# Kernel tuning notes

Hardware: AMD Instinct MI355X
Metric: run time of the kernel (lower is better)

Reference implementation:

```python
import jax, jax.numpy as jnp
import numpy as np

EPS_D = 1e-12  # clamp for sqrt of pairwise distances (diag is exactly 0)


def tr2dist_small(Y):
    # Y: (B, k, N) -> (B, N, N); standard protein-folding coords->distance map
    k = Y.shape[1]
    Z = Y - jnp.mean(Y, axis=2, keepdims=True)
    n2 = jnp.sum(Z * Z, axis=1)                        # (B, N)
    D = n2[:, None, :] + n2[:, :, None] - 2.0 * jnp.einsum('bkn,bkm->bnm', Z, Z)
    D = 3.0 * D / k
    return jnp.sqrt(jnp.maximum(D, EPS_D))


def mean_masked(X, mask, axis, keepdims=True):
    return jnp.sum(X * mask, axis=axis, keepdims=keepdims) / jnp.sum(mask, axis=axis, keepdims=keepdims)


def get_graph_lap(X, mask):
    # X: (B, C, N), mask: (B, 1, N)
    B, C, N = X.shape
    mm = jnp.einsum('bin,bim->bnm', mask, mask)        # (B, N, N) pair mask
    X = X - mean_masked(X, mask, axis=2) * mask
    X = X / jnp.sqrt(jnp.sum(X * X, axis=2, keepdims=True) / jnp.sum(mask, axis=2, keepdims=True) + 1e-4)
    pos = 0.5 * jnp.linspace(0.0, 1.0, N)[None, :] * mask   # (B, 1, N)
    Xa = jnp.concatenate((X, pos), axis=1)
    Wd = tr2dist_small(Xa) * mm
    sigma = mean_masked(Wd, mm, axis=(1, 2))           # (B, 1, 1)
    Wd = jnp.exp(-Wd / sigma * 10.0) * mm
    Wsum = jnp.sum(Wd, axis=1)                         # (B, N)
    L = jnp.zeros_like(Wd) + Wsum[:, :, None] * jnp.eye(N, dtype=Wd.dtype)[None] - Wd
    L = 0.5 * (L + jnp.swapaxes(L, 1, 2))
    return L, Wd


def _forward(Z, mask, K0, Knet, W, Wend):
    h = 0.01
    m = mask[:, None, :]                               # (B, 1, N)
    Z = jnp.tanh(jnp.einsum('oc,bcn->bon', K0, Z)) * m
    nlayers = W.shape[0]
    for i in range(nlayers):
        L, _ = get_graph_lap(Z, m)
        Ki = Knet[i]
        Wi = W[i, :, :, :, 0]                          # (3, C, C) size-1 kernels
        cv = lambda w, x: jnp.einsum('oc,bcn->bon', w, x) * m     # conv1d, k=1
        cvT = lambda w, x: jnp.einsum('co,bcn->bon', w, x) * m    # conv_transpose1d, k=1
        mm1 = lambda x: jnp.einsum('bcn,bnm->bcm', x, L)
        Ai = Ki[0] * cv(Wi[0], Z) + mm1(Ki[1] * cv(Wi[1], Z)) + mm1(mm1(Ki[2] * cv(Wi[2], Z)))
        Ai = (Ai - mean_masked(Ai, m, axis=2)) * m
        Ai = Ai / jnp.sqrt(jnp.sum(Ai * Ai, axis=1, keepdims=True) + 0.001)
        Ai = jax.nn.relu(Ai)
        Ai = Ki[0] * cvT(Wi[0], Ai) + mm1(Ki[1] * cvT(Wi[1], Ai)) + mm1(mm1(Ki[2] * cvT(Wi[2], Ai)))
        Z = Z - h * Ai
    Zout = jnp.einsum('oc,bcn->bon', Wend[:, :, 0], Z) * m       # (B, chan_out, N)
    dists = tuple(tr2dist_small(Zout[:, 3 * i:3 * i + 3, :]) for i in range(Zout.shape[1] // 3))
    return dists + (Zout,)


def setup_inputs() -> dict:
    key = jax.random.key(0)
    ks = jax.random.split(key, 6)
    B, chan_in, chan_out, channels, N, nlayers = 16, 40, 3, 256, 1024, 6
    stdv0 = 0.1 * channels / chan_in
    return {
        'Z': jax.random.normal(ks[0], (B, chan_in, N), dtype=jnp.float32),
        'mask': jnp.ones((B, N), dtype=jnp.float32),
        'K0': jax.random.uniform(ks[1], (channels, chan_in), minval=-stdv0, maxval=stdv0, dtype=jnp.float32),
        'Knet': jax.random.uniform(ks[2], (nlayers, chan_out), minval=-stdv0, maxval=stdv0, dtype=jnp.float32),
        'W': jax.random.uniform(ks[3], (nlayers, 3, channels, channels, 1), minval=-0.1, maxval=0.1, dtype=jnp.float32),
        'Wend': 1e-4 * jax.random.normal(ks[4], (chan_out, channels, 1), dtype=jnp.float32),
    }


def reference(Z, mask, K0, Knet, W, Wend):
    return _forward(Z, mask, K0, Knet, W, Wend)
```

## Files before the change

kernel.cpp:

```cpp
#include <hip/hip_runtime.h>
#include <hip/hip_fp16.h>
#include <math.h>

#define BB 16
#define CIN 40
#define CH 256
#define NN 1024
#define NLAYERS 6

typedef unsigned short ush;
typedef __attribute__((ext_vector_type(8))) short bh8;
typedef __attribute__((ext_vector_type(8))) _Float16 h8;
typedef __attribute__((ext_vector_type(4))) float f4;

__device__ __forceinline__ ush bf16_rne(float x) {
  unsigned int u = __float_as_uint(x);
  u += 0x7fffu + ((u >> 16) & 1u);
  return (ush)(u >> 16);
}
__device__ __forceinline__ float bf16_f(ush h) {
  return __uint_as_float(((unsigned int)h) << 16);
}
__device__ __forceinline__ ush f2h(float x) {
  __half h = __float2half(x);
  return *(ush*)&h;
}
__device__ __forceinline__ float h2f(ush u) {
  __half h = *(__half*)&u;
  return __half2float(h);
}
__device__ __forceinline__ float fast_tanh(float x) {
  const float e = __expf(2.0f * x);
  return (e - 1.0f) / (e + 1.0f);
}

#define GLD16(gp, lp) __builtin_amdgcn_global_load_lds( \
    (const __attribute__((address_space(1))) void*)(gp), \
    (__attribute__((address_space(3))) void*)(lp), 16, 0, 0)

__device__ __forceinline__ float blockReduceSum(float v) {
  __shared__ float sred[4];
  const int lane = threadIdx.x & 63;
  const int wid  = threadIdx.x >> 6;
  #pragma unroll
  for (int off = 32; off > 0; off >>= 1) v += __shfl_down(v, off, 64);
  __syncthreads();
  if (lane == 0) sred[wid] = v;
  __syncthreads();
  return sred[0] + sred[1] + sred[2] + sred[3];
}

__device__ __forceinline__ void stageA(
    const ush* __restrict__ Ah, const ush* __restrict__ Al, const int sA,
    const ush* __restrict__ Bh, const ush* __restrict__ Bl, const int sB,
    const int kt, ush* buf) {
  const int lane = threadIdx.x & 63;
  const int wid = threadIdx.x >> 6;
  const int srow = lane >> 2;
  const int sl = (lane & 3) ^ ((srow >> 1) & 3);
  #pragma unroll
  for (int cc = 0; cc < 8; cc++) {
    const int c = wid * 8 + cc;
    const ush* src;
    if (c < 8)       src = Ah + (size_t)(c * 16 + srow) * sA + kt + sl * 8;
    else if (c < 16) src = Al + (size_t)((c - 8) * 16 + srow) * sA + kt + sl * 8;
    else if (c < 24) src = Bh + (size_t)((c - 16) * 16 + srow) * sB + kt + sl * 8;
    else             src = Bl + (size_t)((c - 24) * 16 + srow) * sB + kt + sl * 8;
    GLD16(src, buf + c * 512 + lane * 8);
  }
}

__device__ __forceinline__ void computeA(const ush* buf, f4 acc[4][4]) {
  const int lane = threadIdx.x & 63;
  const int wid = threadIdx.x >> 6;
  const int wr = wid >> 1, wc = wid & 1;
  const int frow = lane & 15;
  const int slot8 = (((lane >> 4) ^ ((frow >> 1) & 3)) << 3);
  bh8 ah[4], al[4], bh_[4], bl_[4];
  #pragma unroll
  for (int mi = 0; mi < 4; mi++) {
    const int off = (wr * 64 + mi * 16 + frow) * 32 + slot8;
    ah[mi] = *(const bh8*)&buf[off];
    al[mi] = *(const bh8*)&buf[4096 + off];
  }
  #pragma unroll
  for (int ni = 0; ni < 4; ni++) {
    const int off = (wc * 64 + ni * 16 + frow) * 32 + slot8;
    bh_[ni] = *(const bh8*)&buf[8192 + off];
    bl_[ni] = *(const bh8*)&buf[12288 + off];
  }
  #pragma unroll
  for (int mi = 0; mi < 4; mi++)
    #pragma unroll
    for (int ni = 0; ni < 4; ni++) {
      acc[mi][ni] = __builtin_amdgcn_mfma_f32_16x16x32_bf16(ah[mi], bh_[ni], acc[mi][ni], 0, 0, 0);
      acc[mi][ni] = __builtin_amdgcn_mfma_f32_16x16x32_bf16(ah[mi], bl_[ni], acc[mi][ni], 0, 0, 0);
      acc[mi][ni] = __builtin_amdgcn_mfma_f32_16x16x32_bf16(al[mi], bh_[ni], acc[mi][ni], 0, 0, 0);
    }
}

__device__ __forceinline__ void stageCV(
    const ush* __restrict__ Ap, const int sA,
    const ush* __restrict__ Bh, const ush* __restrict__ Bl, const int sB,
    const int kt, ush* buf) {
  const int lane = threadIdx.x & 63;
  const int wid = threadIdx.x >> 6;
  const int srow = lane >> 2;
  const int sl = (lane & 3) ^ ((srow >> 1) & 3);
  #pragma unroll
  for (int cc = 0; cc < 6; cc++) {
    const int c = wid * 6 + cc;
    const ush* src;
    if (c < 8)       src = Ap + (size_t)(c * 16 + srow) * sA + kt + sl * 8;
    else if (c < 16) src = Bh + (size_t)((c - 8) * 16 + srow) * sB + kt + sl * 8;
    else             src = Bl + (size_t)((c - 16) * 16 + srow) * sB + kt + sl * 8;
    GLD16(src, buf + c * 512 + lane * 8);
  }
}

__device__ __forceinline__ void computeCV(const ush* buf, f4 acc[4][4]) {
  const int lane = threadIdx.x & 63;
  const int wid = threadIdx.x >> 6;
  const int wr = wid >> 1, wc = wid & 1;
  const int frow = lane & 15;
  const int slot8 = (((lane >> 4) ^ ((frow >> 1) & 3)) << 3);
  h8 a_[4], bh_[4], bl_[4];
  #pragma unroll
  for (int mi = 0; mi < 4; mi++) {
    const int off = (wr * 64 + mi * 16 + frow) * 32 + slot8;
    a_[mi] = *(const h8*)&buf[off];
  }
  #pragma unroll
  for (int ni = 0; ni < 4; ni++) {
    const int off = (wc * 64 + ni * 16 + frow) * 32 + slot8;
    bh_[ni] = *(const h8*)&buf[4096 + off];
    bl_[ni] = *(const h8*)&buf[8192 + off];
  }
  #pragma unroll
  for (int mi = 0; mi < 4; mi++)
    #pragma unroll
    for (int ni = 0; ni < 4; ni++) {
      acc[mi][ni] = __builtin_amdgcn_mfma_f32_16x16x32_f16(a_[mi], bh_[ni], acc[mi][ni], 0, 0, 0);
      acc[mi][ni] = __builtin_amdgcn_mfma_f32_16x16x32_f16(a_[mi], bl_[ni], acc[mi][ni], 0, 0, 0);
    }
}

__device__ __forceinline__ void stageMM(
    const ush* __restrict__ Ah, const ush* __restrict__ Al, const int sA,
    const ush* __restrict__ Bp, const int sB, const int kt, ush* buf) {
  const int lane = threadIdx.x & 63;
  const int wid = threadIdx.x >> 6;
  const int srow = lane >> 2;
  const int sl = (lane & 3) ^ ((srow >> 1) & 3);
  #pragma unroll
  for (int cc = 0; cc < 4; cc++) {
    const int c = wid * 4 + cc;
    const ush* src;
    if (c < 4)       src = Ah + (size_t)(c * 16 + srow) * sA + kt + sl * 8;
    else if (c < 8)  src = Al + (size_t)((c - 4) * 16 + srow) * sA + kt + sl * 8;
    else             src = Bp + (size_t)((c - 8) * 16 + srow) * sB + kt + sl * 8;
    GLD16(src, buf + c * 512 + lane * 8);
  }
}

__device__ __forceinline__ void computeMM(const ush* buf, f4 acc[4][2]) {
  const int lane = threadIdx.x & 63;
  const int wid = threadIdx.x >> 6;
  const int frow = lane & 15;
  const int slot8 = (((lane >> 4) ^ ((frow >> 1) & 3)) << 3);
  h8 ah[4], al[4], b_[2];
  #pragma unroll
  for (int mi = 0; mi < 4; mi++) {
    const int off = (mi * 16 + frow) * 32 + slot8;
    ah[mi] = *(const h8*)&buf[off];
    al[mi] = *(const h8*)&buf[2048 + off];
  }
  #pragma unroll
  for (int ni = 0; ni < 2; ni++) {
    const int off = (wid * 32 + ni * 16 + frow) * 32 + slot8;
    b_[ni] = *(const h8*)&buf[4096 + off];
  }
  #pragma unroll
  for (int mi = 0; mi < 4; mi++)
    #pragma unroll
    for (int ni = 0; ni < 2; ni++) {
      acc[mi][ni] = __builtin_amdgcn_mfma_f32_16x16x32_f16(ah[mi], b_[ni], acc[mi][ni], 0, 0, 0);
      acc[mi][ni] = __builtin_amdgcn_mfma_f32_16x16x32_f16(al[mi], b_[ni], acc[mi][ni], 0, 0, 0);
    }
}

__global__ void k0_kernel(const float* __restrict__ Zin, const float* __restrict__ K0,
                          const float* __restrict__ mask, float* __restrict__ Zc,
                          float* __restrict__ statS1, float* __restrict__ statS2) {
  const int b = blockIdx.y;
  const int o = blockIdx.x;
  __shared__ float w[CIN];
  if (threadIdx.x < CIN) w[threadIdx.x] = K0[o * CIN + threadIdx.x];
  __syncthreads();
  float s1 = 0.f, s2 = 0.f;
  for (int n = threadIdx.x; n < NN; n += 256) {
    float acc = 0.f;
    #pragma unroll
    for (int c = 0; c < CIN; c++) acc += w[c] * Zin[((size_t)b * CIN + c) * NN + n];
    const float z = fast_tanh(acc) * mask[b * NN + n];
    Zc[((size_t)b * CH + o) * NN + n] = z;
    s1 += z; s2 += z * z;
  }
  s1 = blockReduceSum(s1);
  s2 = blockReduceSum(s2);
  if (threadIdx.x == 0) {
    const size_t base = ((size_t)b * CH + o) * 8;
    statS1[base] = s1; statS2[base] = s2;
    #pragma unroll
    for (int k = 1; k < 8; k++) { statS1[base + k] = 0.f; statS2[base + k] = 0.f; }
  }
}

__global__ void masksum_kernel(const float* __restrict__ mask, float* __restrict__ msum,
                               float* __restrict__ posv) {
  const int b = blockIdx.x;
  float v = 0.f, p = 0.f;
  for (int n = threadIdx.x; n < NN; n += 256) {
    const float m = mask[b * NN + n];
    v += m;
    p += 0.5f * ((float)n * (1.0f / (NN - 1))) * m;
  }
  v = blockReduceSum(v);
  p = blockReduceSum(p);
  const float pm = p * (1.0f / NN);
  if (threadIdx.x == 0) msum[b] = v;
  for (int n = threadIdx.x; n < NN; n += 256)
    posv[b * NN + n] = 0.5f * ((float)n * (1.0f / (NN - 1))) * mask[b * NN + n] - pm;
}

__global__ void wprep_kernel(const float* __restrict__ W, ush* __restrict__ Wm,
                             ush* __restrict__ Wt) {
  __shared__ float t[64][65];
  const int mat = blockIdx.y;
  const int ty = blockIdx.x >> 2, tx = blockIdx.x & 3;
  const float* src = W + (size_t)mat * CH * CH;
  const int tid = threadIdx.x;
  const int lr = tid >> 2;
  const int lc = (tid & 3) * 16;
  float v[16];
  #pragma unroll
  for (int j = 0; j < 16; j += 4)
    *(float4*)&v[j] = *(const float4*)&src[(size_t)(ty * 64 + lr) * CH + tx * 64 + lc + j];
  ush hv[16];
  #pragma unroll
  for (int j = 0; j < 16; j++) {
    hv[j] = f2h(v[j]);
    t[lr][lc + j] = v[j];
  }
  const size_t offm = (size_t)mat * CH * CH + (size_t)(ty * 64 + lr) * CH + tx * 64 + lc;
  #pragma unroll
  for (int j = 0; j < 16; j += 4)
    *(ushort4*)&Wm[offm + j] = *(ushort4*)&hv[j];
  __syncthreads();
  #pragma unroll
  for (int j = 0; j < 16; j++) hv[j] = f2h(t[lc + j][lr]);
  const size_t offt = (size_t)mat * CH * CH + (size_t)(tx * 64 + lr) * CH + ty * 64 + lc;
  #pragma unroll
  for (int j = 0; j < 16; j += 4)
    *(ushort4*)&Wt[offt + j] = *(ushort4*)&hv[j];
}

__global__ void tsplitZ_kernel(const float* __restrict__ in, ush* __restrict__ Th,
                               ush* __restrict__ Tl) {
  __shared__ float t[32][65];
  const int b = blockIdx.z;
  const int n0 = blockIdx.x * 64;
  const int k0 = blockIdx.y * 32;
  const float* src = in + (size_t)b * CH * NN;
  const int tid = threadIdx.x;
  const int lr = tid >> 3;
  const int lc = (tid & 7) * 8;
  const int gk = k0 + lr;
  *(float4*)&t[lr][lc]     = *(const float4*)&src[(size_t)gk * NN + n0 + lc];
  *(float4*)&t[lr][lc + 4] = *(const float4*)&src[(size_t)gk * NN + n0 + lc + 4];
  __syncthreads();
  const int on = tid >> 2;
  const int ok = (tid & 3) * 8;
  ush hv[8], lv[8];
  #pragma unroll
  for (int j = 0; j < 8; j++) {
    const float v = t[ok + j][on];
    hv[j] = f2h(v); lv[j] = f2h(v - h2f(hv[j]));
  }
  const size_t off = ((size_t)b * NN + n0 + on) * CH + k0 + ok;
  *(ushort4*)&Th[off] = *(ushort4*)&hv[0];
  *(ushort4*)&Th[off + 4] = *(ushort4*)&hv[4];
  *(ushort4*)&Tl[off] = *(ushort4*)&lv[0];
  *(ushort4*)&Tl[off + 4] = *(ushort4*)&lv[4];
}

__global__ void tsplitY2_kernel(const ush* __restrict__ Zsh, const ush* __restrict__ Zsl,
                                const float* __restrict__ mask,
                                const float* __restrict__ statS1, const float* __restrict__ statS2,
                                const float* __restrict__ msum, ush* __restrict__ Th,
                                ush* __restrict__ Tl, float* __restrict__ n2part) {
  __shared__ float smu[32], srs[32];
  const int b = blockIdx.z;
  const int n0 = blockIdx.x * 64;
  const int k0 = blockIdx.y * 32;
  const int tid = threadIdx.x;
  if (tid < 32) {
    const size_t base = ((size_t)b * CH + k0 + tid) * 8;
    float S1 = 0.f, S2 = 0.f;
    #pragma unroll
    for (int k = 0; k < 8; k++) { S1 += statS1[base + k]; S2 += statS2[base + k]; }
    const float M = msum[b];
    const float mu = S1 / M;
    const float q = fmaxf(S2 - mu * S1, 0.f);
    smu[tid] = mu;
    srs[tid] = 1.0f / sqrtf(q / M + 1e-4f);
  }
  __syncthreads();
  const int n = n0 + (tid >> 2);
  const int kl = (tid & 3) * 8;
  const int kc = k0 + kl;
  const float mn = mask[b * NN + n];
  const size_t zoff = ((size_t)b * NN + n) * CH + kc;
  const ushort4 h0 = *(const ushort4*)&Zsh[zoff];
  const ushort4 h1 = *(const ushort4*)&Zsh[zoff + 4];
  const ushort4 l0 = *(const ushort4*)&Zsl[zoff];
  const ushort4 l1 = *(const ushort4*)&Zsl[zoff + 4];
  float val[8];
  val[0] = (h2f(h0.x) + h2f(l0.x) - smu[kl + 0] * mn) * srs[kl + 0];
  val[1] = (h2f(h0.y) + h2f(l0.y) - smu[kl + 1] * mn) * srs[kl + 1];
  val[2] = (h2f(h0.z) + h2f(l0.z) - smu[kl + 2] * mn) * srs[kl + 2];
  val[3] = (h2f(h0.w) + h2f(l0.w) - smu[kl + 3] * mn) * srs[kl + 3];
  val[4] = (h2f(h1.x) + h2f(l1.x) - smu[kl + 4] * mn) * srs[kl + 4];
  val[5] = (h2f(h1.y) + h2f(l1.y) - smu[kl + 5] * mn) * srs[kl + 5];
  val[6] = (h2f(h1.z) + h2f(l1.z) - smu[kl + 6] * mn) * srs[kl + 6];
  val[7] = (h2f(h1.w) + h2f(l1.w) - smu[kl + 7] * mn) * srs[kl + 7];
  float s = 0.f;
  ush hv[8], lv[8];
  #pragma unroll
  for (int j = 0; j < 8; j++) {
    s += val[j] * val[j];
    hv[j] = bf16_rne(val[j]);
    lv[j] = bf16_rne(val[j] - bf16_f(hv[j]));
  }
  const size_t off = ((size_t)b * NN + n) * CH + kc;
  *(ushort4*)&Th[off] = *(ushort4*)&hv[0];
  *(ushort4*)&Th[off + 4] = *(ushort4*)&hv[4];
  *(ushort4*)&Tl[off] = *(ushort4*)&lv[0];
  *(ushort4*)&Tl[off + 4] = *(ushort4*)&lv[4];
  s += __shfl_xor(s, 1, 64);
  s += __shfl_xor(s, 2, 64);
  if ((tid & 3) == 0) n2part[((size_t)b * 8 + blockIdx.y) * NN + n] = s;
}

__global__ __launch_bounds__(256, 2)
void gram_v6_kernel(const ush* __restrict__ Yth, const ush* __restrict__ Ytl,
                    const float* __restrict__ n2part, const float* __restrict__ mask,
                    const float* __restrict__ posv, ush* __restrict__ Dp,
                    float* __restrict__ sigpart) {
  __shared__ ush lds[32768];
  __shared__ float sn2[256];
  __shared__ float spv[256];
  const int bid = blockIdx.x;
  const int logical = (bid & 7) * 72 + (bid >> 3);
  const int b = logical / 36;
  int t = logical - b * 36;
  int ty = 0;
  while (t >= 8 - ty) { t -= 8 - ty; ++ty; }
  const int tx = ty + t;
  const int i0 = ty * 128;
  const int j0 = tx * 128;
  {
    const int tt = threadIdx.x;
    const int nn = (tt < 128) ? (i0 + tt) : (j0 + tt - 128);
    const float pv = posv[b * NN + nn];
    float s = pv * pv;
    #pragma unroll
    for (int kb = 0; kb < 8; kb++) s += n2part[((size_t)b * 8 + kb) * NN + nn];
    sn2[tt] = s;
    spv[tt] = pv;
  }
  const ush* Ah = Yth + (size_t)b * NN * CH + (size_t)i0 * CH;
  const ush* Al = Ytl + (size_t)b * NN * CH + (size_t)i0 * CH;
  const ush* Bh = Yth + (size_t)b * NN * CH + (size_t)j0 * CH;
  const ush* Bl = Ytl + (size_t)b * NN * CH + (size_t)j0 * CH;
  f4 acc[4][4];
  const f4 z4 = {0.f, 0.f, 0.f, 0.f};
  #pragma unroll
  for (int mi = 0; mi < 4; mi++)
    #pragma unroll
    for (int ni = 0; ni < 4; ni++) acc[mi][ni] = z4;
  stageA(Ah, Al, CH, Bh, Bl, CH, 0, lds);
  __syncthreads();
  int pb = 0;
  for (int kt = 32; kt < CH; kt += 32) {
    stageA(Ah, Al, CH, Bh, Bl, CH, kt, lds + (pb ^ 1) * 16384);
    computeA(lds + pb * 16384, acc);
    __syncthreads();
    pb ^= 1;
  }
  computeA(lds + pb * 16384, acc);
  const int lane = threadIdx.x & 63;
  const int wid = threadIdx.x >> 6;
  const int wr = wid >> 1, wc = wid & 1;
  const int frow = lane & 15, hh = lane >> 4;
  const float scale = 3.0f / 257.0f;
  float lsum = 0.f;
  #pragma unroll
  for (int ni = 0; ni < 4; ni++) {
    const int jl = wc * 64 + ni * 16 + frow;
    const int j = j0 + jl;
    const float n2j = sn2[128 + jl];
    const float pj = spv[128 + jl];
    const float mkj = mask[b * NN + j];
    #pragma unroll
    for (int mi = 0; mi < 4; mi++) {
      const int il = wr * 64 + mi * 16 + hh * 4;
      ush dv[4];
      #pragma unroll
      for (int r = 0; r < 4; r++) {
        const int i = i0 + il + r;
        const float g = acc[mi][ni][r] + spv[il + r] * pj;
        const float D = scale * (sn2[il + r] + n2j - 2.0f * g);
        const float d = sqrtf(fmaxf(D, 1e-12f));
        const float mmv = mask[b * NN + i] * mkj;
        const float wd = d * mmv;
        lsum += wd * mmv;
        dv[r] = f2h(wd);
      }
      if (ty != tx) {
        uint2 mr;
        mr.x = (unsigned)dv[0] | ((unsigned)dv[1] << 16);
        mr.y = (unsigned)dv[2] | ((unsigned)dv[3] << 16);
        *(uint2*)&Dp[((size_t)b * NN + j) * NN + i0 + il] = mr;
      }
      #pragma unroll
      for (int r = 0; r < 4; r++) {
        const unsigned v = dv[r];
        const unsigned vp = (unsigned)__shfl_xor((int)v, 1, 64);
        if ((frow & 1) == 0)
          *(unsigned*)&Dp[((size_t)b * NN + i0 + il + r) * NN + j] = v | (vp << 16);
      }
    }
  }
  if (ty != tx) lsum *= 2.0f;
  #pragma unroll
  for (int off = 32; off > 0; off >>= 1) lsum += __shfl_down(lsum, off, 64);
  __syncthreads();
  float* rbuf = (float*)lds;
  if (lane == 0) rbuf[wid] = lsum;
  __syncthreads();
  if (threadIdx.x == 0)
    sigpart[(size_t)b * 64 + ty * 8 + tx] = rbuf[0] + rbuf[1] + rbuf[2] + rbuf[3];
}

__global__ void expw4_kernel(const ush* __restrict__ Dp, const float* __restrict__ mask,
                             const float* __restrict__ sigpart, const float* __restrict__ msum,
                             ush* __restrict__ Wp) {
  __shared__ float sfb;
  const int b = blockIdx.y, n = blockIdx.x;
  const int t = threadIdx.x;
  {
    float v = 0.f;
    if (t < 64) {
      const int sy = t >> 3, sx = t & 7;
      if (sy <= sx) v = sigpart[b * 64 + t];
    }
    v = blockReduceSum(v);
    if (t == 0) { const float ms = msum[b]; sfb = -10.0f * ms * ms / v; }
  }
  __syncthreads();
  const float fb = sfb;
  const float mn = mask[b * NN + n];
  const size_t roff = ((size_t)b * NN + n) * NN;
  const float4 mk = ((const float4*)(mask + b * NN))[t];
  const ushort4 dp = *(const ushort4*)&Dp[roff + t * 4];
  const float w0 = __expf(fb * h2f(dp.x)) * mn * mk.x;
  const float w1 = __expf(fb * h2f(dp.y)) * mn * mk.y;
  const float w2 = __expf(fb * h2f(dp.z)) * mn * mk.z;
  const float w3 = __expf(fb * h2f(dp.w)) * mn * mk.w;
  const float s = blockReduceSum(w0 + w1 + w2 + w3);
  float v0 = -w0, v1 = -w1, v2 = -w2, v3 = -w3;
  if ((n >> 2) == t) {
    const int r = n & 3;
    if (r == 0) v0 += s; else if (r == 1) v1 += s; else if (r == 2) v2 += s; else v3 += s;
  }
  ushort4 h4;
  h4.x = f2h(v0); h4.y = f2h(v1); h4.z = f2h(v2); h4.w = f2h(v3);
  *(ushort4*)&Wp[roff + t * 4] = h4;
}

__global__ __launch_bounds__(256, 3)
void cvall_kernel(const ush* __restrict__ Ap, const ush* __restrict__ Bth,
                  const ush* __restrict__ Btl, const float* __restrict__ mask,
                  const float* __restrict__ Kis, unsigned int* __restrict__ Cpack,
                  ush* __restrict__ C2h, ush* __restrict__ C2l) {
  __shared__ ush lds[24576];
  const int bid = blockIdx.x;
  const int logical = (bid & 7) * 96 + (bid >> 3);
  const int b = logical / 48;
  const int inner = logical - b * 48;
  const int c0g = inner & 7;
  const int r0g = inner >> 3;
  const int r0 = r0g * 128;
  const int c0 = c0g * 128;
  const ush* Aq = Ap + (size_t)r0 * CH;
  const ush* Bh = Bth + (size_t)b * NN * CH + (size_t)c0 * CH;
  const ush* Bl = Btl + (size_t)b * NN * CH + (size_t)c0 * CH;
  f4 acc[4][4];
  const f4 z4 = {0.f, 0.f, 0.f, 0.f};
  #pragma unroll
  for (int mi = 0; mi < 4; mi++)
    #pragma unroll
    for (int ni = 0; ni < 4; ni++) acc[mi][ni] = z4;
  stageCV(Aq, CH, Bh, Bl, CH, 0, lds);
  __syncthreads();
  int pb = 0;
  for (int kt = 32; kt < CH; kt += 32) {
    stageCV(Aq, CH, Bh, Bl, CH, kt, lds + (pb ^ 1) * 12288);
    computeCV(lds + pb * 12288, acc);
    __syncthreads();
    pb ^= 1;
  }
  computeCV(lds + pb * 12288, acc);
  const int lane = threadIdx.x & 63;
  const int wid = threadIdx.x >> 6;
  const int wr = wid >> 1, wc = wid & 1;
  const int frow = lane & 15, hh = lane >> 4;
  const float alpha = Kis[r0g >> 1];
  #pragma unroll
  for (int ni = 0; ni < 4; ni++) {
    const int jl = wc * 64 + ni * 16 + frow;
    const int col = c0 + jl;
    const float am = alpha * mask[b * NN + col];
    #pragma unroll
    for (int mi = 0; mi < 4; mi++) {
      const int il = wr * 64 + mi * 16 + hh * 4;
      #pragma unroll
      for (int r = 0; r < 4; r++) {
        const int row = r0 + il + r;
        const float v = acc[mi][ni][r] * am;
        const ush h = f2h(v);
        const ush l = f2h(v - h2f(h));
        const unsigned pv = (unsigned)h | ((unsigned)l << 16);
        const unsigned pvp = (unsigned)__shfl_xor((int)pv, 1, 64);
        if ((frow & 1) == 0) {
          if (r0g < 4) {
            uint2 w2; w2.x = pv; w2.y = pvp;
            *(uint2*)&Cpack[((size_t)b * 512 + row) * NN + col] = w2;
          } else {
            const size_t obase = ((size_t)b * 256 + (row - 512)) * NN + col;
            const unsigned hw = (pv & 0xffffu) | (pvp << 16);
            const unsigned lw = (pv >> 16) | (pvp & 0xffff0000u);
            *(unsigned*)&C2h[obase] = hw;
            *(unsigned*)&C2l[obase] = lw;
          }
        }
      }
    }
  }
}

template <int OUTMODE, int STATS>
__global__ __launch_bounds__(256, 5)
void mm1_v6_kernel(const ush* __restrict__ Xh, const ush* __restrict__ Xl, const size_t xStride,
                   const ush* __restrict__ Wp,
                   const unsigned int* __restrict__ addp, const size_t aStride,
                   const float* __restrict__ zin, const float* __restrict__ mask,
                   float* __restrict__ outF, ush* __restrict__ outH, ush* __restrict__ outL,
                   float* __restrict__ statS1, float* __restrict__ statS2) {
  __shared__ ush lds[16384];
  const int bid = blockIdx.x;
  const int logical = (bid & 7) * 64 + (bid >> 3);
  const int b = logical >> 5;
  const int inner = logical & 31;
  const int n0 = (inner & 7) * 128;
  const int r0 = (inner >> 3) * 64;
  const ush* Ah = Xh + (size_t)b * xStride + (size_t)r0 * NN;
  const ush* Al = Xl + (size_t)b * xStride + (size_t)r0 * NN;
  const ush* Bp = Wp + (size_t)b * NN * NN + (size_t)n0 * NN;
  f4 acc[4][2];
  const f4 z4 = {0.f, 0.f, 0.f, 0.f};
  #pragma unroll
  for (int mi = 0; mi < 4; mi++) { acc[mi][0] = z4; acc[mi][1] = z4; }
  stageMM(Ah, Al, NN, Bp, NN, 0, lds);
  __syncthreads();
  int pb = 0;
  for (int kt = 32; kt < NN; kt += 32) {
    stageMM(Ah, Al, NN, Bp, NN, kt, lds + (pb ^ 1) * 8192);
    computeMM(lds + pb * 8192, acc);
    __syncthreads();
    pb ^= 1;
  }
  computeMM(lds + pb * 8192, acc);
  const int lane = threadIdx.x & 63;
  const int wid = threadIdx.x >> 6;
  const int frow = lane & 15, hh = lane >> 4;
  float a1[4][4];
  float a2[4][4];
  if (STATS) {
    #pragma unroll
    for (int mi = 0; mi < 4; mi++)
      #pragma unroll
      for (int r = 0; r < 4; r++) { a1[mi][r] = 0.f; a2[mi][r] = 0.f; }
  }
  __syncthreads();
  unsigned int* tl = (unsigned int*)lds;
  #pragma unroll
  for (int ni = 0; ni < 2; ni++) {
    const int jl = wid * 32 + ni * 16 + frow;
    const int col = n0 + jl;
    const float mk = STATS ? mask[b * NN + col] : 0.f;
    #pragma unroll
    for (int mi = 0; mi < 4; mi++) {
      const int il = mi * 16 + hh * 4;
      unsigned int pv[4];
      #pragma unroll
      for (int r = 0; r < 4; r++) {
        const int row = r0 + il + r;
        const unsigned int av = addp[(size_t)b * aStride + (size_t)row * NN + col];
        const float o = acc[mi][ni][r] + h2f((ush)(av & 0xffffu)) + h2f((ush)(av >> 16));
        float val;
        if (OUTMODE == 2) {
          const size_t ooff = (size_t)b * CH * NN + (size_t)row * NN + col;
          val = zin[ooff] - 0.01f * o;
          outF[ooff] = val;
        } else {
          val = o;
        }
        if (STATS) { a1[mi][r] += val * mk; a2[mi][r] += val * val * mk; }
        const ush h = f2h(val);
        const ush l = f2h(val - h2f(h));
        pv[r] = (unsigned int)h | ((unsigned int)l << 16);
      }
      const int slot = (il >> 2) ^ (jl & 15);
      *(uint4*)&tl[jl * 64 + slot * 4] = *(uint4*)pv;
    }
  }
  __syncthreads();
  if (OUTMODE == 0) {
    const int rrow = threadIdx.x >> 2;
    const int rch = (threadIdx.x & 3) * 32;
    const size_t obase = ((size_t)b * 256 + r0 + rrow) * NN + n0 + rch;
    #pragma unroll
    for (int g = 0; g < 4; g++) {
      unsigned int hw[4], lw[4];
      #pragma unroll
      for (int q = 0; q < 4; q++) {
        unsigned int h2[2], l2[2];
        #pragma unroll
        for (int e = 0; e < 2; e++) {
          const int jl = rch + g * 8 + q * 2 + e;
          const int slot = (rrow >> 2) ^ (jl & 15);
          const unsigned int v = tl[jl * 64 + slot * 4 + (rrow & 3)];
          h2[e] = v & 0xffffu; l2[e] = v >> 16;
        }
        hw[q] = h2[0] | (h2[1] << 16);
        lw[q] = l2[0] | (l2[1] << 16);
      }
      *(uint4*)&outH[obase + g * 8] = *(uint4*)hw;
      *(uint4*)&outL[obase + g * 8] = *(uint4*)lw;
    }
  } else {
    const int nloc = threadIdx.x >> 1;
    const int ch0 = (threadIdx.x & 1) * 32;
    #pragma unroll
    for (int half = 0; half < 2; half++) {
      unsigned int hw[8], lw[8];
      #pragma unroll
      for (int q = 0; q < 8; q++) {
        const int ila = ch0 + half * 16 + q * 2;
        const int ilb = ila + 1;
        const unsigned int va = tl[nloc * 64 + (((ila >> 2) ^ (nloc & 15)) << 2) + (ila & 3)];
        const unsigned int vb = tl[nloc * 64 + (((ilb >> 2) ^ (nloc & 15)) << 2) + (ilb & 3)];
        hw[q] = (va & 0xffffu) | (vb << 16);
        lw[q] = (va >> 16) | (vb & 0xffff0000u);
      }
      const size_t zoff = ((size_t)b * NN + n0 + nloc) * CH + r0 + ch0 + half * 16;
      *(uint4*)&outH[zoff] = *(uint4*)&hw[0];
      *(uint4*)&outH[zoff + 8] = *(uint4*)&hw[4];
      *(uint4*)&outL[zoff] = *(uint4*)&lw[0];
      *(uint4*)&outL[zoff + 8] = *(uint4*)&lw[4];
    }
  }
  if (STATS) {
    #pragma unroll
    for (int mi = 0; mi < 4; mi++)
      #pragma unroll
      for (int r = 0; r < 4; r++) {
        #pragma unroll
        for (int d = 1; d < 16; d <<= 1) {
          a1[mi][r] += __shfl_xor(a1[mi][r], d, 64);
          a2[mi][r] += __shfl_xor(a2[mi][r], d, 64);
        }
      }
    __syncthreads();
    float* s1b = (float*)lds;
    float* s2b = s1b + 256;
    if (frow == 0) {
      #pragma unroll
      for (int mi = 0; mi < 4; mi++)
        #pragma unroll
        for (int r = 0; r < 4; r++) {
          const int row = mi * 16 + hh * 4 + r;
          s1b[wid * 64 + row] = a1[mi][r];
          s2b[wid * 64 + row] = a2[mi][r];
        }
    }
    __syncthreads();
    if (threadIdx.x < 64) {
      const int row = threadIdx.x;
      const float p1 = s1b[row] + s1b[64 + row] + s1b[128 + row] + s1b[192 + row];
      const float p2 = s2b[row] + s2b[64 + row] + s2b[128 + row] + s2b[192 + row];
      const int nblk = n0 >> 7;
      statS1[((size_t)b * CH + r0 + row) * 8 + nblk] = p1;
      statS2[((size_t)b * CH + r0 + row) * 8 + nblk] = p2;
    }
  }
}

__global__ void csq_kernel(const ush* __restrict__ Uh, const ush* __restrict__ Ul,
                           const float* __restrict__ mask, const float* __restrict__ statS1,
                           const float* __restrict__ msum, float* __restrict__ part) {
  __shared__ float srm[16];
  const int b = blockIdx.y, cc = blockIdx.x;
  if (threadIdx.x < 16) {
    const size_t base = ((size_t)b * CH + cc * 16 + threadIdx.x) * 8;
    float S1 = 0.f;
    #pragma unroll
    for (int k = 0; k < 8; k++) S1 += statS1[base + k];
    srm[threadIdx.x] = S1 / msum[b];
  }
  __syncthreads();
  const int n = threadIdx.x * 4;
  const float4 m4 = *(const float4*)&mask[b * NN + n];
  float4 s4 = {0.f, 0.f, 0.f, 0.f};
  for (int r = 0; r < 16; r++) {
    const int c = cc * 16 + r;
    const float rm = srm[r];
    const size_t uoff = ((size_t)b * 256 + c) * NN + n;
    const ushort4 uh = *(const ushort4*)&Uh[uoff];
    const ushort4 ul = *(const ushort4*)&Ul[uoff];
    float a;
    a = (h2f(uh.x) + h2f(ul.x) - rm) * m4.x; s4.x += a * a;
    a = (h2f(uh.y) + h2f(ul.y) - rm) * m4.y; s4.y += a * a;
    a = (h2f(uh.z) + h2f(ul.z) - rm) * m4.z; s4.z += a * a;
    a = (h2f(uh.w) + h2f(ul.w) - rm) * m4.w; s4.w += a * a;
  }
  *(float4*)&part[((size_t)(b * 16 + cc)) * NN + n] = s4;
}

__global__ void tsplitN2_kernel(const ush* __restrict__ Uh, const ush* __restrict__ Ul,
                                const float* __restrict__ mask, const float* __restrict__ statS1,
                                const float* __restrict__ msum, const float* __restrict__ part,
                                ush* __restrict__ Th, ush* __restrict__ Tl) {
  __shared__ float t[32][65];
  __shared__ float srm[32];
  __shared__ float srsl[64];
  const int b = blockIdx.z;
  const int n0 = blockIdx.x * 64;
  const int k0 = blockIdx.y * 32;
  const int tid = threadIdx.x;
  if (tid < 32) {
    const size_t base = ((size_t)b * CH + k0 + tid) * 8;
    float S1 = 0.f;
    #pragma unroll
    for (int k = 0; k < 8; k++) S1 += statS1[base + k];
    srm[tid] = S1 / msum[b];
  } else if (tid < 96) {
    const int n = n0 + tid - 32;
    float s = 0.001f;
    #pragma unroll
    for (int cc = 0; cc < 16; cc++) s += part[((size_t)(b * 16 + cc)) * NN + n];
    srsl[tid - 32] = 1.0f / sqrtf(s);
  }
  __syncthreads();
  const int lr = tid >> 3;
  const int lc = (tid & 7) * 8;
  const int gc = k0 + lr;
  const float rm = srm[lr];
  const float4 ma = *(const float4*)&mask[b * NN + n0 + lc];
  const float4 mb = *(const float4*)&mask[b * NN + n0 + lc + 4];
  const size_t uoff = ((size_t)b * 256 + gc) * NN + n0 + lc;
  const ushort4 ha = *(const ushort4*)&Uh[uoff];
  const ushort4 hb = *(const ushort4*)&Uh[uoff + 4];
  const ushort4 la = *(const ushort4*)&Ul[uoff];
  const ushort4 lb = *(const ushort4*)&Ul[uoff + 4];
  t[lr][lc + 0] = fmaxf((h2f(ha.x) + h2f(la.x) - rm) * ma.x * srsl[lc + 0], 0.f);
  t[lr][lc + 1] = fmaxf((h2f(ha.y) + h2f(la.y) - rm) * ma.y * srsl[lc + 1], 0.f);
  t[lr][lc + 2] = fmaxf((h2f(ha.z) + h2f(la.z) - rm) * ma.z * srsl[lc + 2], 0.f);
  t[lr][lc + 3] = fmaxf((h2f(ha.w) + h2f(la.w) - rm) * ma.w * srsl[lc + 3], 0.f);
  t[lr][lc + 4] = fmaxf((h2f(hb.x) + h2f(lb.x) - rm) * mb.x * srsl[lc + 4], 0.f);
  t[lr][lc + 5] = fmaxf((h2f(hb.y) + h2f(lb.y) - rm) * mb.y * srsl[lc + 5], 0.f);
  t[lr][lc + 6] = fmaxf((h2f(hb.z) + h2f(lb.z) - rm) * mb.z * srsl[lc + 6], 0.f);
  t[lr][lc + 7] = fmaxf((h2f(hb.w) + h2f(lb.w) - rm) * mb.w * srsl[lc + 7], 0.f);
  __syncthreads();
  const int on = tid >> 2;
  const int ok = (tid & 3) * 8;
  ush hv[8], lv[8];
  #pragma unroll
  for (int j = 0; j < 8; j++) {
    const float v = t[ok + j][on];
    hv[j] = f2h(v); lv[j] = f2h(v - h2f(hv[j]));
  }
  const size_t off = ((size_t)b * NN + n0 + on) * CH + k0 + ok;
  *(ushort4*)&Th[off] = *(ushort4*)&hv[0];
  *(ushort4*)&Th[off + 4] = *(ushort4*)&hv[4];
  *(ushort4*)&Tl[off] = *(ushort4*)&lv[0];
  *(ushort4*)&Tl[off + 4] = *(ushort4*)&lv[4];
}

__global__ void zout_kernel(const float* __restrict__ Z, const float* __restrict__ Wend,
                            const float* __restrict__ mask, float* __restrict__ outZ,
                            float* __restrict__ Zcent) {
  const int b = blockIdx.x;
  __shared__ float w[3 * CH];
  for (int i = threadIdx.x; i < 3 * CH; i += 256) w[i] = Wend[i];
  __syncthreads();
  float a[3][4];
  #pragma unroll
  for (int j = 0; j < 4; j++) { a[0][j] = 0.f; a[1][j] = 0.f; a[2][j] = 0.f; }
  const float* Zb = Z + (size_t)b * CH * NN;
  for (int c = 0; c < CH; c++) {
    const float w0 = w[c], w1 = w[CH + c], w2 = w[2 * CH + c];
    #pragma unroll
    for (int j = 0; j < 4; j++) {
      float zv = Zb[(size_t)c * NN + threadIdx.x + j * 256];
      a[0][j] += w0 * zv; a[1][j] += w1 * zv; a[2][j] += w2 * zv;
    }
  }
  float sum[3] = {0.f, 0.f, 0.f};
  #pragma unroll
  for (int j = 0; j < 4; j++) {
    const int n = threadIdx.x + j * 256;
    const float mv = mask[b * NN + n];
    #pragma unroll
    for (int o = 0; o < 3; o++) {
      a[o][j] *= mv;
      outZ[((size_t)b * 3 + o) * NN + n] = a[o][j];
      sum[o] += a[o][j];
    }
  }
  for (int o = 0; o < 3; o++) {
    float s = blockReduceSum(sum[o]);
    const float mean = s * (1.0f / NN);
    #pragma unroll
    for (int j = 0; j < 4; j++) {
      const int n = threadIdx.x + j * 256;
      Zcent[((size_t)b * 3 + o) * NN + n] = a[o][j] - mean;
    }
  }
}

__global__ void dist_kernel(const float* __restrict__ Zcent, float* __restrict__ outD) {
  const int b = blockIdx.z;
  const int n = blockIdx.y;
  const int m = blockIdx.x * 256 + threadIdx.x;
  const float* Zb = Zcent + (size_t)b * 3 * NN;
  const float x0 = Zb[n], x1 = Zb[NN + n], x2 = Zb[2 * NN + n];
  const float d0 = x0 - Zb[m], d1 = x1 - Zb[NN + m], d2 = x2 - Zb[2 * NN + m];
  const float D = d0 * d0 + d1 * d1 + d2 * d2;
  outD[((size_t)b * NN + n) * NN + m] = sqrtf(fmaxf(D, 1e-12f));
}

extern "C" void kernel_launch(void* const* d_in, const int* in_sizes, int n_in,
                              void* d_out, int out_size, void* d_ws, size_t ws_size,
                              hipStream_t stream) {
  const float* Zin  = (const float*)d_in[0];
  const float* mask = (const float*)d_in[1];
  const float* K0   = (const float*)d_in[2];
  const float* Knet = (const float*)d_in[3];
  const float* W    = (const float*)d_in[4];
  const float* Wend = (const float*)d_in[5];
  float* out = (float*)d_out;

  ush* Wp = (ush*)out;
  ush* Dp = Wp + (size_t)BB * NN * NN;
  float* outZ = out + (size_t)BB * NN * NN;

  float* p = (float*)d_ws;
  float* uni = p; p += (size_t)BB * 768 * NN;
  ush* Yth = (ush*)uni;
  ush* Ytl = Yth + (size_t)BB * NN * CH;
  unsigned int* Cpack = (unsigned int*)uni;
  ush* C2h = (ush*)(uni + (size_t)BB * 512 * NN);
  ush* C2l = C2h + (size_t)BB * 256 * NN;

  float* Zcur = p; p += (size_t)BB * CH * NN;
  ush* Thb = (ush*)p; p += (size_t)BB * NN * CH / 2;
  ush* Tlb = (ush*)p; p += (size_t)BB * NN * CH / 2;
  ush* Zsh = (ush*)p; p += (size_t)BB * NN * CH / 2;
  ush* Zsl = (ush*)p; p += (size_t)BB * NN * CH / 2;
  ush* Wm = (ush*)p; p += (size_t)18 * CH * CH / 2;
  ush* Wt = (ush*)p; p += (size_t)18 * CH * CH / 2;
  float* msum  = p; p += BB;
  float* posv  = p; p += BB * NN;
  float* sigp  = p; p += BB * 64;
  float* statS1= p; p += (size_t)BB * CH * 8;
  float* statS2= p; p += (size_t)BB * CH * 8;
  float* n2part= p; p += (size_t)BB * 8 * NN;
  float* partb = p; p += (size_t)BB * 16 * NN;
  float* Zcent = p; p += BB * 3 * NN;

  const dim3 gtsZ(NN / 64, CH / 32, BB);
  const size_t sC = (size_t)512 * NN;
  const size_t sT = (size_t)CH * NN;

  masksum_kernel<<<BB, 256, 0, stream>>>(mask, msum, posv);
  wprep_kernel<<<dim3(16, 18), 256, 0, stream>>>(W, Wm, Wt);
  k0_kernel<<<dim3(CH, BB), 256, 0, stream>>>(Zin, K0, mask, Zcur, statS1, statS2);
  tsplitZ_kernel<<<gtsZ, 256, 0, stream>>>(Zcur, Zsh, Zsl);

  for (int layer = 0; layer < NLAYERS; layer++) {
    tsplitY2_kernel<<<gtsZ, 256, 0, stream>>>(Zsh, Zsl, mask, statS1, statS2, msum,
                                              Yth, Ytl, n2part);
    gram_v6_kernel<<<576, 256, 0, stream>>>(Yth, Ytl, n2part, mask, posv, Dp, sigp);
    expw4_kernel<<<dim3(NN, BB), 256, 0, stream>>>(Dp, mask, sigp, msum, Wp);

    const ush* Am = Wm + (size_t)layer * 3 * CH * CH;
    const ush* At = Wt + (size_t)layer * 3 * CH * CH;
    const float* Ki = Knet + layer * 3;

    cvall_kernel<<<768, 256, 0, stream>>>(Am, Zsh, Zsl, mask, Ki, Cpack, C2h, C2l);
    mm1_v6_kernel<0, 0><<<512, 256, 0, stream>>>(C2h, C2l, sT, Wp,
        Cpack + (size_t)256 * NN, sC, nullptr, nullptr, nullptr, Thb, Tlb, nullptr, nullptr);
    mm1_v6_kernel<0, 1><<<512, 256, 0, stream>>>(Thb, Tlb, sT, Wp,
        Cpack, sC, nullptr, mask, nullptr, C2h, C2l, statS1, statS2);

    csq_kernel<<<dim3(16, BB), 256, 0, stream>>>(C2h, C2l, mask, statS1, msum, partb);
    tsplitN2_kernel<<<gtsZ, 256, 0, stream>>>(C2h, C2l, mask, statS1, msum, partb, Thb, Tlb);

    cvall_kernel<<<768, 256, 0, stream>>>(At, Thb, Tlb, mask, Ki, Cpack, C2h, C2l);
    mm1_v6_kernel<0, 0><<<512, 256, 0, stream>>>(C2h, C2l, sT, Wp,
        Cpack + (size_t)256 * NN, sC, nullptr, nullptr, nullptr, Thb, Tlb, nullptr, nullptr);
    mm1_v6_kernel<2, 1><<<512, 256, 0, stream>>>(Thb, Tlb, sT, Wp,
        Cpack, sC, Zcur, mask, Zcur, Zsh, Zsl, statS1, statS2);
  }

  zout_kernel<<<BB, 256, 0, stream>>>(Zcur, Wend, mask, outZ, Zcent);
  dist_kernel<<<dim3(NN / 256, NN, BB), 256, 0, stream>>>(Zcent, out);
}
```

Baseline: 1.770 ms.

## Use fp16 hi/lo split for Gram kernel, drop low B term; batch k0 outputs

```diff
diff --git a/kernel.cpp b/kernel.cpp
--- a/kernel.cpp
+++ b/kernel.cpp
@@ -13,14 +13,6 @@
 typedef __attribute__((ext_vector_type(8))) _Float16 h8;
 typedef __attribute__((ext_vector_type(4))) float f4;
 
-__device__ __forceinline__ ush bf16_rne(float x) {
-  unsigned int u = __float_as_uint(x);
-  u += 0x7fffu + ((u >> 16) & 1u);
-  return (ush)(u >> 16);
-}
-__device__ __forceinline__ float bf16_f(ush h) {
-  return __uint_as_float(((unsigned int)h) << 16);
-}
 __device__ __forceinline__ ush f2h(float x) {
   __half h = __float2half(x);
   return *(ush*)&h;
@@ -50,52 +42,48 @@
   return sred[0] + sred[1] + sred[2] + sred[3];
 }
 
-__device__ __forceinline__ void stageA(
-    const ush* __restrict__ Ah, const ush* __restrict__ Al, const int sA,
-    const ush* __restrict__ Bh, const ush* __restrict__ Bl, const int sB,
-    const int kt, ush* buf) {
+__device__ __forceinline__ void stageG(
+    const ush* __restrict__ Ah, const ush* __restrict__ Al,
+    const ush* __restrict__ Bh, const int s, const int kt, ush* buf) {
   const int lane = threadIdx.x & 63;
   const int wid = threadIdx.x >> 6;
   const int srow = lane >> 2;
   const int sl = (lane & 3) ^ ((srow >> 1) & 3);
   #pragma unroll
-  for (int cc = 0; cc < 8; cc++) {
-    const int c = wid * 8 + cc;
+  for (int cc = 0; cc < 6; cc++) {
+    const int c = wid * 6 + cc;
     const ush* src;
-    if (c < 8)       src = Ah + (size_t)(c * 16 + srow) * sA + kt + sl * 8;
-    else if (c < 16) src = Al + (size_t)((c - 8) * 16 + srow) * sA + kt + sl * 8;
-    else if (c < 24) src = Bh + (size_t)((c - 16) * 16 + srow) * sB + kt + sl * 8;
-    else             src = Bl + (size_t)((c - 24) * 16 + srow) * sB + kt + sl * 8;
+    if (c < 8)       src = Ah + (size_t)(c * 16 + srow) * s + kt + sl * 8;
+    else if (c < 16) src = Al + (size_t)((c - 8) * 16 + srow) * s + kt + sl * 8;
+    else             src = Bh + (size_t)((c - 16) * 16 + srow) * s + kt + sl * 8;
     GLD16(src, buf + c * 512 + lane * 8);
   }
 }
 
-__device__ __forceinline__ void computeA(const ush* buf, f4 acc[4][4]) {
+__device__ __forceinline__ void computeG(const ush* buf, f4 acc[4][4]) {
   const int lane = threadIdx.x & 63;
   const int wid = threadIdx.x >> 6;
   const int wr = wid >> 1, wc = wid & 1;
   const int frow = lane & 15;
   const int slot8 = (((lane >> 4) ^ ((frow >> 1) & 3)) << 3);
-  bh8 ah[4], al[4], bh_[4], bl_[4];
+  h8 ah[4], al[4], b_[4];
   #pragma unroll
   for (int mi = 0; mi < 4; mi++) {
     const int off = (wr * 64 + mi * 16 + frow) * 32 + slot8;
-    ah[mi] = *(const bh8*)&buf[off];
-    al[mi] = *(const bh8*)&buf[4096 + off];
+    ah[mi] = *(const h8*)&buf[off];
+    al[mi] = *(const h8*)&buf[4096 + off];
   }
   #pragma unroll
   for (int ni = 0; ni < 4; ni++) {
     const int off = (wc * 64 + ni * 16 + frow) * 32 + slot8;
-    bh_[ni] = *(const bh8*)&buf[8192 + off];
-    bl_[ni] = *(const bh8*)&buf[12288 + off];
+    b_[ni] = *(const h8*)&buf[8192 + off];
   }
   #pragma unroll
   for (int mi = 0; mi < 4; mi++)
     #pragma unroll
     for (int ni = 0; ni < 4; ni++) {
-      acc[mi][ni] = __builtin_amdgcn_mfma_f32_16x16x32_bf16(ah[mi], bh_[ni], acc[mi][ni], 0, 0, 0);
-      acc[mi][ni] = __builtin_amdgcn_mfma_f32_16x16x32_bf16(ah[mi], bl_[ni], acc[mi][ni], 0, 0, 0);
-      acc[mi][ni] = __builtin_amdgcn_mfma_f32_16x16x32_bf16(al[mi], bh_[ni], acc[mi][ni], 0, 0, 0);
+      acc[mi][ni] = __builtin_amdgcn_mfma_f32_16x16x32_f16(ah[mi], b_[ni], acc[mi][ni], 0, 0, 0);
+      acc[mi][ni] = __builtin_amdgcn_mfma_f32_16x16x32_f16(al[mi], b_[ni], acc[mi][ni], 0, 0, 0);
     }
 }
 
@@ -193,26 +181,38 @@
                           const float* __restrict__ mask, float* __restrict__ Zc,
                           float* __restrict__ statS1, float* __restrict__ statS2) {
   const int b = blockIdx.y;
-  const int o = blockIdx.x;
-  __shared__ float w[CIN];
-  if (threadIdx.x < CIN) w[threadIdx.x] = K0[o * CIN + threadIdx.x];
-  __syncthreads();
-  float s1 = 0.f, s2 = 0.f;
+  const int o0 = blockIdx.x * 8;
+  __shared__ float w[8][CIN];
+  for (int i = threadIdx.x; i < 8 * CIN; i += 256)
+    w[i / CIN][i % CIN] = K0[(o0 + i / CIN) * CIN + i % CIN];
+  __syncthreads();
+  float s1[8], s2[8];
+  #pragma unroll
+  for (int o = 0; o < 8; o++) { s1[o] = 0.f; s2[o] = 0.f; }
   for (int n = threadIdx.x; n < NN; n += 256) {
-    float acc = 0.f;
-    #pragma unroll
-    for (int c = 0; c < CIN; c++) acc += w[c] * Zin[((size_t)b * CIN + c) * NN + n];
-    const float z = fast_tanh(acc) * mask[b * NN + n];
-    Zc[((size_t)b * CH + o) * NN + n] = z;
-    s1 += z; s2 += z * z;
-  }
-  s1 = blockReduceSum(s1);
-  s2 = blockReduceSum(s2);
-  if (threadIdx.x == 0) {
-    const size_t base = ((size_t)b * CH + o) * 8;
-    statS1[base] = s1; statS2[base] = s2;
-    #pragma unroll
-    for (int k = 1; k < 8; k++) { statS1[base + k] = 0.f; statS2[base + k] = 0.f; }
+    float zv[CIN];
+    #pragma unroll
+    for (int c = 0; c < CIN; c++) zv[c] = Zin[((size_t)b * CIN + c) * NN + n];
+    const float mn = mask[b * NN + n];
+    #pragma unroll
+    for (int o = 0; o < 8; o++) {
+      float acc = 0.f;
+      #pragma unroll
+      for (int c = 0; c < CIN; c++) acc += w[o][c] * zv[c];
+      const float z = fast_tanh(acc) * mn;
+      Zc[((size_t)b * CH + o0 + o) * NN + n] = z;
+      s1[o] += z; s2[o] += z * z;
+    }
+  }
+  for (int o = 0; o < 8; o++) {
+    const float r1 = blockReduceSum(s1[o]);
+    const float r2 = blockReduceSum(s2[o]);
+    if (threadIdx.x == 0) {
+      const size_t base = ((size_t)b * CH + o0 + o) * 8;
+      statS1[base] = r1; statS2[base] = r2;
+      #pragma unroll
+      for (int k = 1; k < 8; k++) { statS1[base + k] = 0.f; statS2[base + k] = 0.f; }
+    }
   }
 }
 
@@ -339,8 +339,8 @@
   #pragma unroll
   for (int j = 0; j < 8; j++) {
     s += val[j] * val[j];
-    hv[j] = bf16_rne(val[j]);
-    lv[j] = bf16_rne(val[j] - bf16_f(hv[j]));
+    hv[j] = f2h(val[j]);
+    lv[j] = f2h(val[j] - h2f(hv[j]));
   }
   const size_t off = ((size_t)b * NN + n) * CH + kc;
   *(ushort4*)&Th[off] = *(ushort4*)&hv[0];
@@ -352,12 +352,12 @@
   if ((tid & 3) == 0) n2part[((size_t)b * 8 + blockIdx.y) * NN + n] = s;
 }
 
-__global__ __launch_bounds__(256, 2)
-void gram_v6_kernel(const ush* __restrict__ Yth, const ush* __restrict__ Ytl,
+__global__ __launch_bounds__(256, 3)
+void gram_v7_kernel(const ush* __restrict__ Yth, const ush* __restrict__ Ytl,
                     const float* __restrict__ n2part, const float* __restrict__ mask,
                     const float* __restrict__ posv, ush* __restrict__ Dp,
                     float* __restrict__ sigpart) {
-  __shared__ ush lds[32768];
+  __shared__ ush lds[24576];
   __shared__ float sn2[256];
   __shared__ float spv[256];
   const int bid = blockIdx.x;
@@ -382,23 +382,22 @@
   const ush* Ah = Yth + (size_t)b * NN * CH + (size_t)i0 * CH;
   const ush* Al = Ytl + (size_t)b * NN * CH + (size_t)i0 * CH;
   const ush* Bh = Yth + (size_t)b * NN * CH + (size_t)j0 * CH;
-  const ush* Bl = Ytl + (size_t)b * NN * CH + (size_t)j0 * CH;
   f4 acc[4][4];
   const f4 z4 = {0.f, 0.f, 0.f, 0.f};
   #pragma unroll
   for (int mi = 0; mi < 4; mi++)
     #pragma unroll
     for (int ni = 0; ni < 4; ni++) acc[mi][ni] = z4;
-  stageA(Ah, Al, CH, Bh, Bl, CH, 0, lds);
+  stageG(Ah, Al, Bh, CH, 0, lds);
   __syncthreads();
   int pb = 0;
   for (int kt = 32; kt < CH; kt += 32) {
-    stageA(Ah, Al, CH, Bh, Bl, CH, kt, lds + (pb ^ 1) * 16384);
-    computeA(lds + pb * 16384, acc);
+    stageG(Ah, Al, Bh, CH, kt, lds + (pb ^ 1) * 12288);
+    computeG(lds + pb * 12288, acc);
     __syncthreads();
     pb ^= 1;
   }
-  computeA(lds + pb * 16384, acc);
+  computeG(lds + pb * 12288, acc);
   const int lane = threadIdx.x & 63;
   const int wid = threadIdx.x >> 6;
   const int wr = wid >> 1, wc = wid & 1;
@@ -907,13 +906,13 @@
 
   masksum_kernel<<<BB, 256, 0, stream>>>(mask, msum, posv);
   wprep_kernel<<<dim3(16, 18), 256, 0, stream>>>(W, Wm, Wt);
-  k0_kernel<<<dim3(CH, BB), 256, 0, stream>>>(Zin, K0, mask, Zcur, statS1, statS2);
+  k0_kernel<<<dim3(CH / 8, BB), 256, 0, stream>>>(Zin, K0, mask, Zcur, statS1, statS2);
   tsplitZ_kernel<<<gtsZ, 256, 0, stream>>>(Zcur, Zsh, Zsl);
 
   for (int layer = 0; layer < NLAYERS; layer++) {
     tsplitY2_kernel<<<gtsZ, 256, 0, stream>>>(Zsh, Zsl, mask, statS1, statS2, msum,
                                               Yth, Ytl, n2part);
-    gram_v6_kernel<<<576, 256, 0, stream>>>(Yth, Ytl, n2part, mask, posv, Dp, sigp);
+    gram_v7_kernel<<<576, 256, 0, stream>>>(Yth, Ytl, n2part, mask, posv, Dp, sigp);
     expw4_kernel<<<dim3(NN, BB), 256, 0, stream>>>(Dp, mask, sigp, msum, Wp);
 
     const ush* Am = Wm + (size_t)layer * 3 * CH * CH;
```

Result: slower. 1.855 ms (+4.8%).
